# Kernel optimization log

Hardware: AMD Instinct MI355X
Metric: run time of the kernel (lower is better)

Reference implementation:

```python
import jax, jax.numpy as jnp
import numpy as np

B, H, W, C = 32, 56, 56, 512
WS, SHIFT, NH = 7, 3, 16
N = WS * WS
NW = (H // WS) * (W // WS)
HID = 4 * C
EPS = 1e-5


def _np_constants():
    # log-spaced relative coords table (SwinV2 CPB input), pretrained_window_size=[0,0]
    rh = np.arange(-(WS - 1), WS, dtype=np.float32)
    tbl = np.stack(np.meshgrid(rh, rh, indexing='ij'), axis=-1)  # (2*WS-1, 2*WS-1, 2)
    tbl = tbl / (WS - 1) * 8.0
    tbl = np.sign(tbl) * np.log2(np.abs(tbl) + 1.0) / np.log2(8.0)
    coords = np.stack(np.meshgrid(np.arange(WS), np.arange(WS), indexing='ij'))
    cf = coords.reshape(2, -1)
    rc = (cf[:, :, None] - cf[:, None, :]).transpose(1, 2, 0).copy()  # (N,N,2)
    rc[..., 0] += WS - 1
    rc[..., 1] += WS - 1
    rc[..., 0] *= 2 * WS - 1
    rpi = rc.sum(-1)  # (N,N) indices into the (2*WS-1)^2 table
    # shifted-window attention mask
    img = np.zeros((H, W), dtype=np.float32)
    sl = (slice(0, -WS), slice(-WS, -SHIFT), slice(-SHIFT, None))
    cnt = 0
    for hs in sl:
        for ws in sl:
            img[hs, ws] = cnt
            cnt += 1
    mw = img.reshape(H // WS, WS, W // WS, WS).transpose(0, 2, 1, 3).reshape(-1, N)
    am = mw[:, None, :] - mw[:, :, None]
    attn_mask = np.where(am != 0, -100.0, 0.0).astype(np.float32)  # (NW,N,N)
    return tbl.reshape(-1, 2).astype(np.float32), rpi.reshape(-1), attn_mask

TBL_NP, RPI_NP, MASK_NP = _np_constants()


def _ln(x, g, b):
    mu = jnp.mean(x, -1, keepdims=True)
    var = jnp.mean((x - mu) ** 2, -1, keepdims=True)
    return (x - mu) * jax.lax.rsqrt(var + EPS) * g + b


def _win_part(x):  # (B,H,W,C) -> (B*NW, N, C)
    x = x.reshape(B, H // WS, WS, W // WS, WS, C).transpose(0, 1, 3, 2, 4, 5)
    return x.reshape(-1, N, C)


def _win_rev(w):  # (B*NW, N, C) -> (B,H,W,C)
    x = w.reshape(B, H // WS, W // WS, WS, WS, C).transpose(0, 1, 3, 2, 4, 5)
    return x.reshape(B, H, W, C)


def setup_inputs() -> dict:
    key = jax.random.key(0)
    ks = jax.random.split(key, 8)
    s = 0.02
    return {
        'x': jax.random.normal(ks[0], (B, H * W, C), jnp.float32),
        'qkv_w': jax.random.normal(ks[1], (3 * C, C), jnp.float32) * s,
        'q_bias': jnp.zeros((C,), jnp.float32),
        'v_bias': jnp.zeros((C,), jnp.float32),
        'logit_scale': jnp.log(10.0) * jnp.ones((NH, 1, 1), jnp.float32),
        'cpb_w1': jax.random.normal(ks[2], (512, 2), jnp.float32) * s,
        'cpb_b1': jnp.zeros((512,), jnp.float32),
        'cpb_w2': jax.random.normal(ks[3], (NH, 512), jnp.float32) * s,
        'proj_w': jax.random.normal(ks[4], (C, C), jnp.float32) * s,
        'proj_b': jnp.zeros((C,), jnp.float32),
        'norm1_g': jnp.ones((C,), jnp.float32),
        'norm1_b': jnp.zeros((C,), jnp.float32),
        'fc1_w': jax.random.normal(ks[5], (HID, C), jnp.float32) * s,
        'fc1_b': jnp.zeros((HID,), jnp.float32),
        'fc2_w': jax.random.normal(ks[6], (C, HID), jnp.float32) * s,
        'fc2_b': jnp.zeros((C,), jnp.float32),
        'norm2_g': jnp.ones((C,), jnp.float32),
        'norm2_b': jnp.zeros((C,), jnp.float32),
    }


def reference(x, qkv_w, q_bias, v_bias, logit_scale, cpb_w1, cpb_b1, cpb_w2,
              proj_w, proj_b, norm1_g, norm1_b, fc1_w, fc1_b, fc2_w, fc2_b,
              norm2_g, norm2_b):
    tbl = jnp.asarray(TBL_NP)
    mask = jnp.asarray(MASK_NP)
    shortcut = x
    xi = x.reshape(B, H, W, C)
    xi = jnp.roll(xi, shift=(-SHIFT, -SHIFT), axis=(1, 2))
    xw = _win_part(xi)  # (B*NW, N, C)
    qkv_bias = jnp.concatenate([q_bias, jnp.zeros_like(v_bias), v_bias])
    qkv = xw @ qkv_w.T + qkv_bias
    qkv = qkv.reshape(-1, N, 3, NH, C // NH).transpose(2, 0, 3, 1, 4)
    q, k, v = qkv[0], qkv[1], qkv[2]  # (B_, NH, N, hd)
    qn = q / jnp.maximum(jnp.linalg.norm(q, axis=-1, keepdims=True), 1e-12)
    kn = k / jnp.maximum(jnp.linalg.norm(k, axis=-1, keepdims=True), 1e-12)
    scale = jnp.exp(jnp.minimum(logit_scale, jnp.log(100.0)))  # (NH,1,1)
    attn = jnp.einsum('bhnd,bhmd->bhnm', qn, kn) * scale
    # CPB MLP -> relative position bias
    hcb = jax.nn.relu(tbl @ cpb_w1.T + cpb_b1)       # (169, 512)
    bias_tbl = hcb @ cpb_w2.T                        # (169, NH)
    rpb = bias_tbl[RPI_NP].reshape(N, N, NH).transpose(2, 0, 1)
    rpb = 16.0 * jax.nn.sigmoid(rpb)
    attn = attn + rpb[None]
    attn = attn.reshape(B, NW, NH, N, N) + mask[None, :, None]
    attn = jax.nn.softmax(attn.reshape(-1, NH, N, N), axis=-1)
    out = jnp.einsum('bhnm,bhmd->bhnd', attn, v).transpose(0, 2, 1, 3).reshape(-1, N, C)
    out = out @ proj_w.T + proj_b
    xi = _win_rev(out)
    xi = jnp.roll(xi, shift=(SHIFT, SHIFT), axis=(1, 2)).reshape(B, H * W, C)
    x = shortcut + _ln(xi, norm1_g, norm1_b)  # SwinV2 post-norm residual
    hmlp = jax.nn.gelu(x @ fc1_w.T + fc1_b, approximate=False)
    m = hmlp @ fc2_w.T + fc2_b
    x = x + _ln(m, norm2_g, norm2_b)
    return x
```

## Files before the change

kernel.cpp:

```cpp
#include <hip/hip_runtime.h>

typedef unsigned short u16;
typedef unsigned int   u32;

using f32x4  = __attribute__((ext_vector_type(4))) float;
using bf16x8 = __attribute__((ext_vector_type(8))) short;

__device__ __forceinline__ float bf2f(u16 u){
  union { u32 i; float f; } x; x.i = ((u32)u) << 16; return x.f;
}
__device__ __forceinline__ u16 f2bf(float f){
  union { float f; u32 i; } x; x.f = f;
  u32 r = x.i + 0x7FFFu + ((x.i >> 16) & 1u);
  return (u16)(r >> 16);
}
__device__ __forceinline__ int pack2(float a, float b){
  return (int)f2bf(a) | ((int)f2bf(b) << 16);
}

__device__ __forceinline__ void glds16(const void* g, void* l){
  __builtin_amdgcn_global_load_lds(
      (const __attribute__((address_space(1))) unsigned int*)g,
      (__attribute__((address_space(3))) unsigned int*)(unsigned int)(unsigned long long)l,
      16, 0, 0);
}

__device__ __forceinline__ int rollmap(int m){
  int win = m / 49, n = m % 49;
  int b  = win >> 6, wi = win & 63;
  int wh = wi >> 3, ww = wi & 7;
  int r = n / 7, c = n % 7;
  int sh = wh*7 + r + 3; if (sh >= 56) sh -= 56;
  int sw = ww*7 + c + 3; if (sw >= 56) sw -= 56;
  return b*3136 + sh*56 + sw;
}

template<int EPI, int AMODE>
__global__ __launch_bounds__(256) void gemm_bt(const void* __restrict__ Ap,
      const u16* __restrict__ Bw, const float* __restrict__ bias,
      void* __restrict__ outp, int M, int N, int K, int nbn)
{
  __shared__ __align__(16) u16 As[128*32];
  __shared__ __align__(16) u16 Bs[128*32];
  const int t    = threadIdx.x;
  const int lane = t & 63, wave = t >> 6;
  const int wm = wave >> 1, wn = wave & 1;

  const int gl = ((blockIdx.x & 7) * ((int)gridDim.x >> 3)) + (blockIdx.x >> 3);
  const int bm = gl / nbn, bn = gl - bm*nbn;

  const int r0 = t >> 2;
  const int sc = t & 3;
  const int dc = sc ^ ((r0 >> 1) & 3);

  const u16* gB0 = Bw + (size_t)(bn*128 + r0)*K + dc*8;
  const u16* gA0_h = nullptr;
  const float* pA0_f = nullptr; const float* pA1_f = nullptr;
  if constexpr (AMODE == 0){
    gA0_h = (const u16*)Ap + (size_t)(bm*128 + r0)*K + dc*8;
  } else {
    const float* A = (const float*)Ap;
    pA0_f = A + (size_t)rollmap(bm*128 + r0     )*512 + sc*8;
    pA1_f = A + (size_t)rollmap(bm*128 + r0 + 64)*512 + sc*8;
  }
  const int sA0 = r0*64 + ((sc ^ ((r0 >> 1) & 3)) * 16);

  const int lr = lane & 15, lk = lane >> 4;
  int offA[4], offB[4];
#pragma unroll
  for (int i = 0; i < 4; ++i){
    int ar = wm*64 + i*16 + lr;
    offA[i] = ar*64 + ((lk ^ ((ar >> 1) & 3)) * 16);
    int br = wn*64 + i*16 + lr;
    offB[i] = br*64 + ((lk ^ ((br >> 1) & 3)) * 16);
  }

  f32x4 acc[4][4];
#pragma unroll
  for (int i = 0; i < 4; ++i)
#pragma unroll
    for (int j = 0; j < 4; ++j) acc[i][j] = (f32x4){0.f, 0.f, 0.f, 0.f};

  char* AsB = (char*)As;
  char* BsB = (char*)Bs;

  for (int kt = 0; kt < K; kt += 32){
    int4 av0, av1;
    if constexpr (AMODE == 1){
      float4 f0 = *(const float4*)(pA0_f + kt);
      float4 f1 = *(const float4*)(pA0_f + kt + 4);
      av0 = make_int4(pack2(f0.x,f0.y), pack2(f0.z,f0.w), pack2(f1.x,f1.y), pack2(f1.z,f1.w));
      float4 g0 = *(const float4*)(pA1_f + kt);
      float4 g1 = *(const float4*)(pA1_f + kt + 4);
      av1 = make_int4(pack2(g0.x,g0.y), pack2(g0.z,g0.w), pack2(g1.x,g1.y), pack2(g1.z,g1.w));
    }
    __syncthreads();
    if constexpr (AMODE == 0){
      glds16(gA0_h + kt,            AsB + wave*1024);
      glds16(gA0_h + kt + 64*K,     AsB + 4096 + wave*1024);
    } else {
      *(int4*)(AsB + sA0)        = av0;
      *(int4*)(AsB + sA0 + 4096) = av1;
    }
    glds16(gB0 + kt,        BsB + wave*1024);
    glds16(gB0 + kt + 64*K, BsB + 4096 + wave*1024);
    __syncthreads();
    bf16x8 fa[4], fb[4];
#pragma unroll
    for (int i = 0; i < 4; ++i){
      fa[i] = *(const bf16x8*)(AsB + offA[i]);
      fb[i] = *(const bf16x8*)(BsB + offB[i]);
    }
#pragma unroll
    for (int i = 0; i < 4; ++i)
#pragma unroll
      for (int j = 0; j < 4; ++j)
        acc[i][j] = __builtin_amdgcn_mfma_f32_16x16x32_bf16(fa[i], fb[j], acc[i][j], 0, 0, 0);
  }

#pragma unroll
  for (int i = 0; i < 4; ++i){
#pragma unroll
    for (int j = 0; j < 4; ++j){
      int cm = bm*128 + wm*64 + i*16 + (lane >> 4)*4;
      int cn = bn*128 + wn*64 + j*16 + (lane & 15);
      float bv = bias[cn];
#pragma unroll
      for (int r = 0; r < 4; ++r){
        float v = acc[i][j][r] + bv;
        if (EPI == 2) v = 0.5f * v * (1.f + erff(v * 0.70710678118f));
        if (EPI == 1) ((float*)outp)[(size_t)(cm + r)*N + cn] = v;
        else          ((u16*)  outp)[(size_t)(cm + r)*N + cn] = f2bf(v);
      }
    }
  }
}

__global__ __launch_bounds__(256, 2) void attn_mfma(const u16* __restrict__ qkv,
      const float* __restrict__ rpb, const float* __restrict__ ls,
      u16* __restrict__ outp)
{
  __shared__ __align__(16) u16 Pl[4][64*72];
  __shared__ __align__(16) u16 Vl[4][32*72];
  __shared__ unsigned char regid[64];
  const int tid  = threadIdx.x, lane = tid & 63, wave = tid >> 6;
  const int lc = lane & 15, lg = lane >> 4;
  const int pair = blockIdx.x*4 + wave;
  const int win = pair >> 4, h = pair & 15;

  const u16* qb = qkv + (size_t)win*49*1536 + h*32;
  const u16* kb = qb + 512;
  const u16* vb = qb + 1024;

  if (tid < 49){
    int wi = win & 63, wh = wi >> 3, ww = wi & 7;
    int q7 = (tid*37) >> 8, r7 = tid - q7*7;
    int gh = wh*7 + q7, gw = ww*7 + r7;
    int rh = gh < 49 ? 0 : (gh < 53 ? 1 : 2);
    int rw = gw < 49 ? 0 : (gw < 53 ? 1 : 2);
    regid[tid] = (unsigned char)(rh*3 + rw);
  }

  u16* V = &Vl[wave][0];
#pragma unroll
  for (int it = 0; it < 4; ++it){
    int ch = it*64 + lane;
    int n = ch >> 2, oct = ch & 3;
    union { int4 i4; u16 s[8]; } v8;
    if (n < 49) v8.i4 = *(const int4*)(vb + (size_t)n*1536 + oct*8);
    else        v8.i4 = make_int4(0,0,0,0);
#pragma unroll
    for (int q = 0; q < 8; ++q) V[(oct*8 + q)*72 + n] = v8.s[q];
  }

  const float scale = __expf(fminf(ls[h], 4.6051702f));
  bf16x8 qf[4], kf[4];
#pragma unroll
  for (int ti = 0; ti < 4; ++ti){
    const int n = ti*16 + lc;
    {
      union { int4 i4; u16 s[8]; } raw;
      raw.i4 = *(const int4*)(qb + (size_t)n*1536 + lg*8);
      float f[8]; float ss = 0.f;
#pragma unroll
      for (int q = 0; q < 8; ++q){ f[q] = bf2f(raw.s[q]); ss += f[q]*f[q]; }
      ss += __shfl_xor(ss, 16); ss += __shfl_xor(ss, 32);
      const float inv = scale / fmaxf(sqrtf(ss), 1e-12f);
      union { short s[8]; bf16x8 v; } o;
#pragma unroll
      for (int q = 0; q < 8; ++q) o.s[q] = (short)f2bf(f[q]*inv);
      qf[ti] = o.v;
    }
    {
      union { int4 i4; u16 s[8]; } raw;
      raw.i4 = *(const int4*)(kb + (size_t)n*1536 + lg*8);
      float f[8]; float ss = 0.f;
#pragma unroll
      for (int q = 0; q < 8; ++q){ f[q] = bf2f(raw.s[q]); ss += f[q]*f[q]; }
      ss += __shfl_xor(ss, 16); ss += __shfl_xor(ss, 32);
      const float inv = 1.f / fmaxf(sqrtf(ss), 1e-12f);
      union { short s[8]; bf16x8 v; } o;
#pragma unroll
      for (int q = 0; q < 8; ++q) o.s[q] = (short)f2bf(f[q]*inv);
      kf[ti] = o.v;
    }
  }
  __syncthreads();

  f32x4 acc[4][4];
#pragma unroll
  for (int i = 0; i < 4; ++i)
#pragma unroll
    for (int j = 0; j < 4; ++j) acc[i][j] = (f32x4){0.f,0.f,0.f,0.f};
#pragma unroll
  for (int i = 0; i < 4; ++i)
#pragma unroll
    for (int j = 0; j < 4; ++j)
      acc[i][j] = __builtin_amdgcn_mfma_f32_16x16x32_bf16(qf[i], kf[j], acc[i][j], 0, 0, 0);

  u16* P = &Pl[wave][0];
  int rj[4];
#pragma unroll
  for (int tj = 0; tj < 4; ++tj){
    int j = tj*16 + lc;
    rj[tj] = (int)regid[j < 49 ? j : 0];
  }
  const float* rpbh = rpb + h*2401;
#pragma unroll
  for (int ti = 0; ti < 4; ++ti){
#pragma unroll
    for (int r = 0; r < 4; ++r){
      const int i = ti*16 + lg*4 + r;
      const bool iv = i < 49;
      const int ic = iv ? i : 0;
      const int ri = (int)regid[ic];
      const float* rrow = rpbh + ic*49;
      float sv[4];
#pragma unroll
      for (int tj = 0; tj < 4; ++tj){
        const int j = tj*16 + lc;
        float t2 = acc[ti][tj][r] + rrow[j < 49 ? j : 0];
        if (ri != rj[tj]) t2 -= 100.f;
        sv[tj] = (iv && j < 49) ? t2 : -1e30f;
      }
      float mx = fmaxf(fmaxf(sv[0],sv[1]), fmaxf(sv[2],sv[3]));
      mx = fmaxf(mx, __shfl_xor(mx, 1));
      mx = fmaxf(mx, __shfl_xor(mx, 2));
      mx = fmaxf(mx, __shfl_xor(mx, 4));
      mx = fmaxf(mx, __shfl_xor(mx, 8));
      float p[4], sum = 0.f;
#pragma unroll
      for (int tj = 0; tj < 4; ++tj){ p[tj] = __expf(sv[tj] - mx); sum += p[tj]; }
      sum += __shfl_xor(sum, 1); sum += __shfl_xor(sum, 2);
      sum += __shfl_xor(sum, 4); sum += __shfl_xor(sum, 8);
      const float rs = __builtin_amdgcn_rcpf(sum);
#pragma unroll
      for (int tj = 0; tj < 4; ++tj) P[i*72 + tj*16 + lc] = f2bf(p[tj]*rs);
    }
  }
  __syncthreads();

  f32x4 o[4][2];
#pragma unroll
  for (int i = 0; i < 4; ++i){ o[i][0] = (f32x4){0.f,0.f,0.f,0.f}; o[i][1] = (f32x4){0.f,0.f,0.f,0.f}; }
#pragma unroll
  for (int ks = 0; ks < 2; ++ks){
    bf16x8 pa[4], vf[2];
#pragma unroll
    for (int ti = 0; ti < 4; ++ti)
      pa[ti] = *(const bf16x8*)((const char*)P + (ti*16 + lc)*144 + (ks*4 + lg)*16);
#pragma unroll
    for (int tc = 0; tc < 2; ++tc)
      vf[tc] = *(const bf16x8*)((const char*)V + (tc*16 + lc)*144 + (ks*4 + lg)*16);
#pragma unroll
    for (int ti = 0; ti < 4; ++ti)
#pragma unroll
      for (int tc = 0; tc < 2; ++tc)
        o[ti][tc] = __builtin_amdgcn_mfma_f32_16x16x32_bf16(pa[ti], vf[tc], o[ti][tc], 0, 0, 0);
  }

#pragma unroll
  for (int ti = 0; ti < 4; ++ti){
#pragma unroll
    for (int tc = 0; tc < 2; ++tc){
#pragma unroll
      for (int r = 0; r < 4; ++r){
        const int i = ti*16 + lg*4 + r;
        if (i < 49)
          outp[((size_t)win*49 + i)*512 + h*32 + tc*16 + lc] = f2bf(o[ti][tc][r]);
      }
    }
  }
}

__global__ __launch_bounds__(256) void ln1_kernel(const float* __restrict__ x,
      const float* __restrict__ y, const float* __restrict__ g, const float* __restrict__ bt,
      float* __restrict__ xout, u16* __restrict__ xbf)
{
  __shared__ float red[8];
  const int t = blockIdx.x;
  const int b = t / 3136, s = t % 3136;
  const int hh = s / 56, ww2 = s % 56;
  int ph = hh + 53; if (ph >= 56) ph -= 56;
  int pw = ww2 + 53; if (pw >= 56) pw -= 56;
  const int win = b*64 + (ph/7)*8 + (pw/7);
  const int n   = (ph%7)*7 + (pw%7);
  const float* yr = y + ((size_t)win*49 + n)*512;
  const int c = threadIdx.x * 2;
  float2 v = *(const float2*)(yr + c);
  float sum = v.x + v.y, sq = v.x*v.x + v.y*v.y;
#pragma unroll
  for (int off = 32; off; off >>= 1){ sum += __shfl_xor(sum, off); sq += __shfl_xor(sq, off); }
  if ((threadIdx.x & 63) == 0){ red[threadIdx.x >> 6] = sum; red[(threadIdx.x >> 6) + 4] = sq; }
  __syncthreads();
  sum = red[0]+red[1]+red[2]+red[3];
  sq  = red[4]+red[5]+red[6]+red[7];
  const float mu  = sum * (1.f/512.f);
  const float inv = rsqrtf(fmaxf(sq * (1.f/512.f) - mu*mu, 0.f) + 1e-5f);
  const float* xr = x + (size_t)t*512;
  float2 xv = *(const float2*)(xr + c);
  float o0 = xv.x + (v.x - mu)*inv*g[c]   + bt[c];
  float o1 = xv.y + (v.y - mu)*inv*g[c+1] + bt[c+1];
  float* orow = xout + (size_t)t*512;
  orow[c] = o0; orow[c+1] = o1;
  *(u32*)(xbf + (size_t)t*512 + c) = (u32)f2bf(o0) | ((u32)f2bf(o1) << 16);
}

__global__ __launch_bounds__(256) void ln2_kernel(const u16* __restrict__ m,
      const float* __restrict__ g, const float* __restrict__ bt, float* __restrict__ out)
{
  __shared__ float red[8];
  const int t = blockIdx.x;
  const int c = threadIdx.x * 2;
  u32 u = *(const u32*)(m + (size_t)t*512 + c);
  float v0 = bf2f((u16)(u & 0xffff)), v1 = bf2f((u16)(u >> 16));
  float sum = v0 + v1, sq = v0*v0 + v1*v1;
#pragma unroll
  for (int off = 32; off; off >>= 1){ sum += __shfl_xor(sum, off); sq += __shfl_xor(sq, off); }
  if ((threadIdx.x & 63) == 0){ red[threadIdx.x >> 6] = sum; red[(threadIdx.x >> 6) + 4] = sq; }
  __syncthreads();
  sum = red[0]+red[1]+red[2]+red[3];
  sq  = red[4]+red[5]+red[6]+red[7];
  const float mu  = sum * (1.f/512.f);
  const float inv = rsqrtf(fmaxf(sq * (1.f/512.f) - mu*mu, 0.f) + 1e-5f);
  float* orow = out + (size_t)t*512;
  orow[c]   += (v0 - mu)*inv*g[c]   + bt[c];
  orow[c+1] += (v1 - mu)*inv*g[c+1] + bt[c+1];
}

__global__ void cast_bf16_kernel(const float* __restrict__ in, u16* __restrict__ out, int n4){
  int i = blockIdx.x*256 + threadIdx.x;
  if (i >= n4) return;
  float4 v = *(const float4*)(in + (size_t)i*4);
  u32 lo = (u32)f2bf(v.x) | ((u32)f2bf(v.y) << 16);
  u32 hi = (u32)f2bf(v.z) | ((u32)f2bf(v.w) << 16);
  *(uint2*)(out + (size_t)i*4) = make_uint2(lo, hi);
}
__global__ void qkvbias_kernel(const float* __restrict__ qb, const float* __restrict__ vb,
                               float* __restrict__ out){
  int i = blockIdx.x*256 + threadIdx.x;
  if (i >= 1536) return;
  out[i] = i < 512 ? qb[i] : (i < 1024 ? 0.f : vb[i - 1024]);
}
__device__ __forceinline__ float cpb_coord(int d){
  float v = (float)(d - 6) * (8.f/6.f);
  float m = log2f(fabsf(v) + 1.f) * (1.f/3.f);
  return v > 0.f ? m : (v < 0.f ? -m : 0.f);
}
__global__ void cpb_kernel(const float* __restrict__ w1, const float* __restrict__ b1,
                           const float* __restrict__ w2, float* __restrict__ btbl){
  int idx = blockIdx.x*256 + threadIdx.x;
  if (idx >= 169*16) return;
  int e = idx >> 4, h = idx & 15;
  float t0 = cpb_coord(e / 13), t1 = cpb_coord(e % 13);
  float acc = 0.f;
  for (int jj = 0; jj < 512; ++jj){
    float hid = fmaxf(t0*w1[jj*2] + t1*w1[jj*2+1] + b1[jj], 0.f);
    acc += hid * w2[h*512 + jj];
  }
  btbl[e*16 + h] = acc;
}
__global__ void rpb_kernel(const float* __restrict__ btbl, float* __restrict__ rpb){
  int idx = blockIdx.x*256 + threadIdx.x;
  if (idx >= 16*49*49) return;
  int hh = idx / 2401, ij = idx % 2401, i = ij / 49, j = ij % 49;
  int dr = i/7 - j/7 + 6, dc = i%7 - j%7 + 6;
  float bb = btbl[(dr*13 + dc)*16 + hh];
  rpb[idx] = 16.f / (1.f + __expf(-bb));
}

extern "C" void kernel_launch(void* const* d_in, const int* in_sizes, int n_in,
                              void* d_out, int out_size, void* d_ws, size_t ws_size,
                              hipStream_t stream)
{
  const float* x    = (const float*)d_in[0];
  const float* qkvw = (const float*)d_in[1];
  const float* qb   = (const float*)d_in[2];
  const float* vb   = (const float*)d_in[3];
  const float* ls   = (const float*)d_in[4];
  const float* cw1  = (const float*)d_in[5];
  const float* cb1  = (const float*)d_in[6];
  const float* cw2  = (const float*)d_in[7];
  const float* pw   = (const float*)d_in[8];
  const float* pb   = (const float*)d_in[9];
  const float* n1g  = (const float*)d_in[10];
  const float* n1b  = (const float*)d_in[11];
  const float* f1w  = (const float*)d_in[12];
  const float* f1b  = (const float*)d_in[13];
  const float* f2w  = (const float*)d_in[14];
  const float* f2b  = (const float*)d_in[15];
  const float* n2g  = (const float*)d_in[16];
  const float* n2b  = (const float*)d_in[17];

  char* ws = (char*)d_ws;
  const size_t SZ_BIG = (size_t)100352 * 2048 * 2;
  const size_t SZ_MID = (size_t)100352 * 512  * 2;
  size_t o = SZ_BIG + SZ_MID;
  u16* wqkv  = (u16*)(ws + o); o += (size_t)1536*512*2;
  u16* wproj = (u16*)(ws + o); o += (size_t)512*512*2;
  u16* wfc1  = (u16*)(ws + o); o += (size_t)2048*512*2;
  u16* wfc2  = (u16*)(ws + o); o += (size_t)512*2048*2;
  float* qkvbias = (float*)(ws + o); o += 1536*4;
  float* btbl    = (float*)(ws + o); o += 2704*4;
  float* rpb     = (float*)(ws + o); o += 38416*4;

  u16*   big_h = (u16*)ws;
  float* y_f   = (float*)ws;
  u16*   mid   = (u16*)(ws + SZ_BIG);
  float* out   = (float*)d_out;

  cast_bf16_kernel<<<768,  256, 0, stream>>>(qkvw, wqkv, 1536*512/4);
  cast_bf16_kernel<<<256,  256, 0, stream>>>(pw,  wproj, 512*512/4);
  cast_bf16_kernel<<<1024, 256, 0, stream>>>(f1w, wfc1, 2048*512/4);
  cast_bf16_kernel<<<1024, 256, 0, stream>>>(f2w, wfc2, 512*2048/4);
  qkvbias_kernel<<<6, 256, 0, stream>>>(qb, vb, qkvbias);
  cpb_kernel<<<11, 256, 0, stream>>>(cw1, cb1, cw2, btbl);
  rpb_kernel<<<151, 256, 0, stream>>>(btbl, rpb);

  gemm_bt<0,1><<<784*12, 256, 0, stream>>>((const void*)x, wqkv, qkvbias,
                                           (void*)big_h, 100352, 1536, 512, 12);
  attn_mfma<<<8192, 256, 0, stream>>>(big_h, rpb, ls, mid);
  gemm_bt<1,0><<<784*4, 256, 0, stream>>>((const void*)mid, wproj, pb,
                                          (void*)y_f, 100352, 512, 512, 4);
  ln1_kernel<<<100352, 256, 0, stream>>>(x, y_f, n1g, n1b, out, mid);
  gemm_bt<2,0><<<784*16, 256, 0, stream>>>((const void*)mid, wfc1, f1b,
                                           (void*)big_h, 100352, 2048, 512, 16);
  gemm_bt<0,0><<<784*4, 256, 0, stream>>>((const void*)big_h, wfc2, f2b,
                                          (void*)mid, 100352, 512, 2048, 4);
  ln2_kernel<<<100352, 256, 0, stream>>>(mid, n2g, n2b, out);
}
```

Baseline: 1.722 ms.

## Pre-cast input to bf16, async-load rolled rows, tanh GELU, bf16 proj output

Adds a bulk cast of x to bf16 so the QKV GEMM can load rolled rows directly into LDS through global_load_lds, instead of converting fp32 to bf16 inside the K loop. The exact erf GELU is replaced with a tanh approximation built on __expf. The projection GEMM now writes bf16 rather than fp32, which halves the write traffic and the bytes ln1 reads. The cost is an extra pass over x to cast it, plus lower precision in the projection output and in GELU.

```diff
diff --git a/kernel.cpp b/kernel.cpp
--- a/kernel.cpp
+++ b/kernel.cpp
@@ -14,8 +14,10 @@
   u32 r = x.i + 0x7FFFu + ((x.i >> 16) & 1u);
   return (u16)(r >> 16);
 }
-__device__ __forceinline__ int pack2(float a, float b){
-  return (int)f2bf(a) | ((int)f2bf(b) << 16);
+__device__ __forceinline__ float gelu_f(float v){
+  float u = 0.7978845608f * v * (1.f + 0.044715f*v*v);
+  float e = __expf(2.f*u);
+  return 0.5f*v*(2.f - 2.f/(e + 1.f));
 }
 
 __device__ __forceinline__ void glds16(const void* g, void* l){
@@ -36,7 +38,7 @@
 }
 
 template<int EPI, int AMODE>
-__global__ __launch_bounds__(256) void gemm_bt(const void* __restrict__ Ap,
+__global__ __launch_bounds__(256) void gemm_bt(const u16* __restrict__ A,
       const u16* __restrict__ Bw, const float* __restrict__ bias,
       void* __restrict__ outp, int M, int N, int K, int nbn)
 {
@@ -54,16 +56,15 @@
   const int dc = sc ^ ((r0 >> 1) & 3);
 
   const u16* gB0 = Bw + (size_t)(bn*128 + r0)*K + dc*8;
-  const u16* gA0_h = nullptr;
-  const float* pA0_f = nullptr; const float* pA1_f = nullptr;
+  const u16* gB1 = gB0 + (size_t)64*K;
+  const u16* gA0; const u16* gA1;
   if constexpr (AMODE == 0){
-    gA0_h = (const u16*)Ap + (size_t)(bm*128 + r0)*K + dc*8;
+    gA0 = A + (size_t)(bm*128 + r0)*K + dc*8;
+    gA1 = gA0 + (size_t)64*K;
   } else {
-    const float* A = (const float*)Ap;
-    pA0_f = A + (size_t)rollmap(bm*128 + r0     )*512 + sc*8;
-    pA1_f = A + (size_t)rollmap(bm*128 + r0 + 64)*512 + sc*8;
-  }
-  const int sA0 = r0*64 + ((sc ^ ((r0 >> 1) & 3)) * 16);
+    gA0 = A + (size_t)rollmap(bm*128 + r0     )*K + dc*8;
+    gA1 = A + (size_t)rollmap(bm*128 + r0 + 64)*K + dc*8;
+  }
 
   const int lr = lane & 15, lk = lane >> 4;
   int offA[4], offB[4];
@@ -85,25 +86,11 @@
   char* BsB = (char*)Bs;
 
   for (int kt = 0; kt < K; kt += 32){
-    int4 av0, av1;
-    if constexpr (AMODE == 1){
-      float4 f0 = *(const float4*)(pA0_f + kt);
-      float4 f1 = *(const float4*)(pA0_f + kt + 4);
-      av0 = make_int4(pack2(f0.x,f0.y), pack2(f0.z,f0.w), pack2(f1.x,f1.y), pack2(f1.z,f1.w));
-      float4 g0 = *(const float4*)(pA1_f + kt);
-      float4 g1 = *(const float4*)(pA1_f + kt + 4);
-      av1 = make_int4(pack2(g0.x,g0.y), pack2(g0.z,g0.w), pack2(g1.x,g1.y), pack2(g1.z,g1.w));
-    }
     __syncthreads();
-    if constexpr (AMODE == 0){
-      glds16(gA0_h + kt,            AsB + wave*1024);
-      glds16(gA0_h + kt + 64*K,     AsB + 4096 + wave*1024);
-    } else {
-      *(int4*)(AsB + sA0)        = av0;
-      *(int4*)(AsB + sA0 + 4096) = av1;
-    }
-    glds16(gB0 + kt,        BsB + wave*1024);
-    glds16(gB0 + kt + 64*K, BsB + 4096 + wave*1024);
+    glds16(gA0 + kt, AsB +        wave*1024);
+    glds16(gA1 + kt, AsB + 4096 + wave*1024);
+    glds16(gB0 + kt, BsB +        wave*1024);
+    glds16(gB1 + kt, BsB + 4096 + wave*1024);
     __syncthreads();
     bf16x8 fa[4], fb[4];
 #pragma unroll
@@ -128,7 +115,7 @@
 #pragma unroll
       for (int r = 0; r < 4; ++r){
         float v = acc[i][j][r] + bv;
-        if (EPI == 2) v = 0.5f * v * (1.f + erff(v * 0.70710678118f));
+        if (EPI == 2) v = gelu_f(v);
         if (EPI == 1) ((float*)outp)[(size_t)(cm + r)*N + cn] = v;
         else          ((u16*)  outp)[(size_t)(cm + r)*N + cn] = f2bf(v);
       }
@@ -294,7 +281,7 @@
 }
 
 __global__ __launch_bounds__(256) void ln1_kernel(const float* __restrict__ x,
-      const float* __restrict__ y, const float* __restrict__ g, const float* __restrict__ bt,
+      const u16* __restrict__ y, const float* __restrict__ g, const float* __restrict__ bt,
       float* __restrict__ xout, u16* __restrict__ xbf)
 {
   __shared__ float red[8];
@@ -305,10 +292,11 @@
   int pw = ww2 + 53; if (pw >= 56) pw -= 56;
   const int win = b*64 + (ph/7)*8 + (pw/7);
   const int n   = (ph%7)*7 + (pw%7);
-  const float* yr = y + ((size_t)win*49 + n)*512;
+  const u16* yr = y + ((size_t)win*49 + n)*512;
   const int c = threadIdx.x * 2;
-  float2 v = *(const float2*)(yr + c);
-  float sum = v.x + v.y, sq = v.x*v.x + v.y*v.y;
+  u32 u = *(const u32*)(yr + c);
+  float vx = bf2f((u16)(u & 0xffff)), vy = bf2f((u16)(u >> 16));
+  float sum = vx + vy, sq = vx*vx + vy*vy;
 #pragma unroll
   for (int off = 32; off; off >>= 1){ sum += __shfl_xor(sum, off); sq += __shfl_xor(sq, off); }
   if ((threadIdx.x & 63) == 0){ red[threadIdx.x >> 6] = sum; red[(threadIdx.x >> 6) + 4] = sq; }
@@ -319,8 +307,8 @@
   const float inv = rsqrtf(fmaxf(sq * (1.f/512.f) - mu*mu, 0.f) + 1e-5f);
   const float* xr = x + (size_t)t*512;
   float2 xv = *(const float2*)(xr + c);
-  float o0 = xv.x + (v.x - mu)*inv*g[c]   + bt[c];
-  float o1 = xv.y + (v.y - mu)*inv*g[c+1] + bt[c+1];
+  float o0 = xv.x + (vx - mu)*inv*g[c]   + bt[c];
+  float o1 = xv.y + (vy - mu)*inv*g[c+1] + bt[c+1];
   float* orow = xout + (size_t)t*512;
   orow[c] = o0; orow[c+1] = o1;
   *(u32*)(xbf + (size_t)t*512 + c) = (u32)f2bf(o0) | ((u32)f2bf(o1) << 16);
@@ -424,8 +412,10 @@
   float* btbl    = (float*)(ws + o); o += 2704*4;
   float* rpb     = (float*)(ws + o); o += 38416*4;
 
+  u16*   xbf   = (u16*)ws;
+  u16*   qkvo  = (u16*)(ws + (size_t)100352*512*2);
+  u16*   y_h   = (u16*)ws;
   u16*   big_h = (u16*)ws;
-  float* y_f   = (float*)ws;
   u16*   mid   = (u16*)(ws + SZ_BIG);
   float* out   = (float*)d_out;
 
@@ -436,16 +426,17 @@
   qkvbias_kernel<<<6, 256, 0, stream>>>(qb, vb, qkvbias);
   cpb_kernel<<<11, 256, 0, stream>>>(cw1, cb1, cw2, btbl);
   rpb_kernel<<<151, 256, 0, stream>>>(btbl, rpb);
-
-  gemm_bt<0,1><<<784*12, 256, 0, stream>>>((const void*)x, wqkv, qkvbias,
-                                           (void*)big_h, 100352, 1536, 512, 12);
-  attn_mfma<<<8192, 256, 0, stream>>>(big_h, rpb, ls, mid);
-  gemm_bt<1,0><<<784*4, 256, 0, stream>>>((const void*)mid, wproj, pb,
-                                          (void*)y_f, 100352, 512, 512, 4);
-  ln1_kernel<<<100352, 256, 0, stream>>>(x, y_f, n1g, n1b, out, mid);
-  gemm_bt<2,0><<<784*16, 256, 0, stream>>>((const void*)mid, wfc1, f1b,
+  cast_bf16_kernel<<<50176, 256, 0, stream>>>(x, xbf, 100352*512/4);
+
+  gemm_bt<0,2><<<784*12, 256, 0, stream>>>(xbf, wqkv, qkvbias,
+                                           (void*)qkvo, 100352, 1536, 512, 12);
+  attn_mfma<<<8192, 256, 0, stream>>>(qkvo, rpb, ls, mid);
+  gemm_bt<0,0><<<784*4, 256, 0, stream>>>(mid, wproj, pb,
+                                          (void*)y_h, 100352, 512, 512, 4);
+  ln1_kernel<<<100352, 256, 0, stream>>>(x, y_h, n1g, n1b, out, mid);
+  gemm_bt<2,0><<<784*16, 256, 0, stream>>>(mid, wfc1, f1b,
                                            (void*)big_h, 100352, 2048, 512, 16);
-  gemm_bt<0,0><<<784*4, 256, 0, stream>>>((const void*)big_h, wfc2, f2b,
+  gemm_bt<0,0><<<784*4, 256, 0, stream>>>(big_h, wfc2, f2b,
                                           (void*)mid, 100352, 512, 2048, 4);
   ln2_kernel<<<100352, 256, 0, stream>>>(mid, n2g, n2b, out);
 }
```

Result: faster. 1.617 ms (-6.1%).
